# Kernel tuning notes

Measured on AMD Instinct MI355X. Metric: run time of the kernel, lower is better.

Reference implementation:

```python
import jax, jax.numpy as jnp
import numpy as np

B, M, T, D, V = 16, 1024, 4096, 512, 32000
HOPS = 2  # multi_layer_gcn layer_number=2


def setup_inputs() -> dict:
    key = jax.random.key(0)
    ks = jax.random.split(key, 10)
    s = 1.0 / np.sqrt(D)
    emb = jax.random.normal(ks[0], (V, D), jnp.float32) * 0.02
    Ws = jax.random.normal(ks[1], (HOPS, D, D), jnp.float32) * s
    Wn = jax.random.normal(ks[2], (HOPS, D, D), jnp.float32) * s
    Wr = jax.random.normal(ks[3], (HOPS, D, D), jnp.float32) * s
    Wt = jax.random.normal(ks[4], (D, 3 * D), jnp.float32) * (1.0 / np.sqrt(3 * D))
    concept_ids = jax.random.randint(ks[5], (B, M), 0, V)
    relation = jax.random.randint(ks[6], (B, T), 0, V)
    head = jax.random.randint(ks[7], (B, T), 0, M)
    tail = jax.random.randint(ks[8], (B, T), 0, M)
    triple_label = jax.random.randint(ks[9], (B, T), -1, 2)  # {-1,0,1}
    return dict(emb=emb, Ws=Ws, Wn=Wn, Wr=Wr, Wt=Wt,
                concept_ids=concept_ids, relation=relation,
                head=head, tail=tail, triple_label=triple_label)


def _forward(emb, Ws, Wn, Wr, Wt, concept_ids, relation, head, tail, triple_label):
    x = emb[concept_ids]        # [B, M, D] node hidden
    rel = emb[relation]         # [B, T, D] relation hidden
    mask = (triple_label != -1).astype(x.dtype)  # [B, T]

    # per-batch scatter_add into M node slots
    scat = jax.vmap(lambda msg, idx: jnp.zeros((M, msg.shape[-1]), msg.dtype).at[idx].add(msg))
    scat1 = jax.vmap(lambda v, idx: jnp.zeros((M,), v.dtype).at[idx].add(v))

    for i in range(HOPS):
        oh = jnp.take_along_axis(x, head[..., None], axis=1) * mask[..., None]  # gather heads
        ot = jnp.take_along_axis(x, tail[..., None], axis=1) * mask[..., None]  # gather tails
        relm = rel * mask[..., None]
        # update_node += scatter(head_repr - rel -> tail) + scatter(tail_repr - rel -> head)
        upd = scat(oh - relm, tail) + scat(ot - relm, head)          # [B, M, D]
        cnt = scat1(mask, tail) + scat1(mask, head)                  # [B, M]
        x = jax.nn.relu(
            jnp.einsum('bmd,ed->bme', x, Ws[i])
            + jnp.einsum('bmd,ed->bme', upd, Wn[i]) / jnp.maximum(cnt, 1.0)[..., None]
        )
        rel = jnp.einsum('btd,ed->bte', rel, Wr[i])

    head_repr = jnp.take_along_axis(x, head[..., None], axis=1)  # [B, T, D]
    tail_repr = jnp.take_along_axis(x, tail[..., None], axis=1)  # [B, T, D]
    triple_repr = jnp.concatenate([head_repr, rel, tail_repr], axis=-1)  # [B, T, 3D]
    triple_repr = jnp.einsum('btk,dk->btd', triple_repr, Wt)     # [B, T, D]
    encoded_cause = triple_repr.sum(axis=1)                      # [B, D]
    return triple_repr, encoded_cause


def reference(emb, Ws, Wn, Wr, Wt, concept_ids, relation, head, tail, triple_label):
    return _forward(emb, Ws, Wn, Wr, Wt, concept_ids, relation, head, tail, triple_label)
```

## Files before the change

kernel.cpp:

```cpp
#include <hip/hip_runtime.h>

namespace {

constexpr int kB = 16;
constexpr int kM = 1024;
constexpr int kT = 4096;
constexpr int kD = 512;
constexpr int kV = 32000;

typedef __attribute__((ext_vector_type(8))) short bfrag8;
typedef __attribute__((ext_vector_type(4))) float f4acc;

__device__ __forceinline__ ushort f2bf(float f) {
  unsigned u = __float_as_uint(f);
  u += 0x7fffu + ((u >> 16) & 1u);
  return (ushort)(u >> 16);
}
__device__ __forceinline__ float bf2f(ushort h) {
  return __uint_as_float(((unsigned)h) << 16);
}

__device__ __forceinline__ void gload_lds16(const void* g, void* l) {
  __builtin_amdgcn_global_load_lds(
      (const __attribute__((address_space(1))) void*)g,
      (__attribute__((address_space(3))) void*)l, 16, 0, 0);
}

constexpr int kN0 = kV * kD / 4;
constexpr int kN1 = kN0 + 2 * kD * kD / 4;
constexpr int kN2 = kN1 + 2 * kD * kD / 4;
constexpr int kN3 = kN2 + kD * 1536 / 4;
constexpr int kN4 = kN3 + kB * kM * 128;
constexpr int kPREPB = kN4 / 1024;
constexpr int kCSRB = 16;
constexpr int kMM2B = 256;

__global__ __launch_bounds__(1024) void fused_prep_k(
    const float4* __restrict__ emb, const float4* __restrict__ Ws,
    const float4* __restrict__ Wn, const float4* __restrict__ Wt,
    const float* __restrict__ Wnf, const float* __restrict__ Wtf,
    const float* __restrict__ Wrf,
    const int* __restrict__ cid,
    const int* __restrict__ headp, const int* __restrict__ tailp,
    const int* __restrict__ lblp,
    ushort4* __restrict__ EMBb, ushort4* __restrict__ Wsb,
    ushort4* __restrict__ Wnb, ushort4* __restrict__ Wtb,
    ushort4* __restrict__ X0,
    int* __restrict__ deg, int* __restrict__ rowstart, int* __restrict__ epack,
    ushort* __restrict__ Wn2r, float* __restrict__ T1)
{
  __shared__ __align__(16) char shm[12288];
  const int bid = blockIdx.x;
  const int tid = threadIdx.x;

  if (bid < kCSRB) {
    int* sdeg = (int*)shm;
    int* sscan = (int*)(shm + 4096);
    int* sfill = (int*)(shm + 8192);
    const int b = bid;
    sdeg[tid] = 0;
    __syncthreads();
    const int* hb = headp + (b << 12);
    const int* tb = tailp + (b << 12);
    const int* lb = lblp + (b << 12);
    for (int t = tid; t < kT; t += 1024) {
      if (lb[t] == -1) continue;
      atomicAdd(&sdeg[tb[t]], 1);
      atomicAdd(&sdeg[hb[t]], 1);
    }
    __syncthreads();
    int d = sdeg[tid];
    sscan[tid] = d;
    __syncthreads();
    for (int off = 1; off < kM; off <<= 1) {
      int add = (tid >= off) ? sscan[tid - off] : 0;
      __syncthreads();
      sscan[tid] += add;
      __syncthreads();
    }
    int rs = b * (2 * kT) + sscan[tid] - d;
    deg[(b << 10) + tid] = d;
    rowstart[(b << 10) + tid] = rs;
    sfill[tid] = rs;
    __syncthreads();
    for (int t = tid; t < kT; t += 1024) {
      if (lb[t] == -1) continue;
      int hd = hb[t];
      int tl = tb[t];
      int p0 = atomicAdd(&sfill[tl], 1);
      epack[p0] = ((t * 2) << 10) | hd;
      int p1 = atomicAdd(&sfill[hd], 1);
      epack[p1] = ((t * 2 + 1) << 10) | tl;
    }
    __syncthreads();
    for (int i = 1; i < d; ++i) {
      int key = epack[rs + i];
      int j = i - 1;
      while (j >= 0 && epack[rs + j] > key) {
        epack[rs + j + 1] = epack[rs + j];
        --j;
      }
      epack[rs + j + 1] = key;
    }
  } else if (bid < kCSRB + kPREPB) {
    int i = (bid - kCSRB) * 1024 + tid;
    if (i >= kN4) return;
    const float4* s;
    ushort4* dP;
    int off;
    if (i < kN0) { s = emb; dP = EMBb; off = i; }
    else if (i < kN1) { s = Ws; dP = Wsb; off = i - kN0; }
    else if (i < kN2) { s = Wn; dP = Wnb; off = i - kN1; }
    else if (i < kN3) { s = Wt; dP = Wtb; off = i - kN2; }
    else {
      int idx = i - kN3;
      int row = idx >> 7;
      int c = idx & 127;
      float4 v = emb[(size_t)cid[row] * 128 + c];
      ushort4 o;
      o.x = f2bf(v.x); o.y = f2bf(v.y); o.z = f2bf(v.z); o.w = f2bf(v.w);
      X0[idx] = o;
      return;
    }
    float4 v = s[off];
    ushort4 o;
    o.x = f2bf(v.x); o.y = f2bf(v.y); o.z = f2bf(v.z); o.w = f2bf(v.w);
    dP[off] = o;
  } else {
    float (*prow)[512] = (float(*)[512])shm;
    const int mb = bid - kCSRB - kPREPB;
    const int job = mb >> 7;
    const int e0 = (mb & 127) * 4;
    const int k = tid & 511;
    const float* P;
    int strideP, offsP;
    const float* Q;
    if (job == 0) { P = Wnf + (size_t)kD * kD; strideP = 512; offsP = 0; Q = Wrf; }
    else { P = Wtf; strideP = 1536; offsP = 512; Q = Wrf + (size_t)kD * kD; }
    if (tid < 512) {
#pragma unroll
      for (int i = 0; i < 4; ++i)
        prow[i][k] = P[(size_t)(e0 + i) * strideP + offsP + k];
    }
    __syncthreads();
    if (tid < 512) {
      float acc[4] = {0.f, 0.f, 0.f, 0.f};
      for (int a = 0; a < 512; ++a) {
        float qv = Q[a * 512 + k];
#pragma unroll
        for (int i = 0; i < 4; ++i) acc[i] = fmaf(prow[i][a], qv, acc[i]);
      }
#pragma unroll
      for (int i = 0; i < 4; ++i) {
        if (job == 0) Wn2r[(e0 + i) * 512 + k] = f2bf(acc[i]);
        else T1[(e0 + i) * 512 + k] = acc[i];
      }
    }
  }
}

constexpr int kFOLDB = 128;

__global__ __launch_bounds__(512) void fold_aggxr_k(
    const float* __restrict__ T1, const float* __restrict__ Wrf,
    ushort* __restrict__ Wfold,
    const ushort4* __restrict__ Xv, const ushort4* __restrict__ EMBv,
    const int* __restrict__ relid,
    const int* __restrict__ deg, const int* __restrict__ rowstart,
    const int* __restrict__ epack,
    ushort4* __restrict__ SxC, ushort4* __restrict__ nSr0n)
{
  __shared__ float prow[4][512];
  const int bid = blockIdx.x;
  const int tid = threadIdx.x;
  if (bid < kFOLDB) {
    int e0 = bid * 4;
    int k = tid;
#pragma unroll
    for (int i = 0; i < 4; ++i)
      prow[i][k] = T1[(size_t)(e0 + i) * 512 + k];
    __syncthreads();
    float acc[4] = {0.f, 0.f, 0.f, 0.f};
    for (int a = 0; a < 512; ++a) {
      float qv = Wrf[a * 512 + k];
#pragma unroll
      for (int i = 0; i < 4; ++i) acc[i] = fmaf(prow[i][a], qv, acc[i]);
    }
#pragma unroll
    for (int i = 0; i < 4; ++i) Wfold[(e0 + i) * 512 + k] = f2bf(acc[i]);
  } else {
    int bm = (bid - kFOLDB) * 4 + (tid >> 7);
    int t128 = tid & 127;
    int b = bm >> 10;
    int dg = deg[bm];
    int rs = rowstart[bm];
    const int* rid = relid + (b << 12);
    size_t xbase = (size_t)b * kM * 128;
    float ax = 0.f, ay = 0.f, az = 0.f, aw = 0.f;
    float rx = 0.f, ry = 0.f, rz = 0.f, rw = 0.f;
    int e = 0;
    for (; e + 4 <= dg; e += 4) {
      int pk[4];
#pragma unroll
      for (int j = 0; j < 4; ++j) pk[j] = epack[rs + e + j];
      ushort4 xv[4], rv[4];
#pragma unroll
      for (int j = 0; j < 4; ++j) {
        xv[j] = Xv[xbase + (size_t)(pk[j] & 1023) * 128 + t128];
        rv[j] = EMBv[(size_t)rid[pk[j] >> 11] * 128 + t128];
      }
#pragma unroll
      for (int j = 0; j < 4; ++j) {
        ax += bf2f(xv[j].x); ay += bf2f(xv[j].y);
        az += bf2f(xv[j].z); aw += bf2f(xv[j].w);
        rx += bf2f(rv[j].x); ry += bf2f(rv[j].y);
        rz += bf2f(rv[j].z); rw += bf2f(rv[j].w);
      }
    }
    for (; e < dg; ++e) {
      int pk = epack[rs + e];
      ushort4 xv = Xv[xbase + (size_t)(pk & 1023) * 128 + t128];
      ushort4 rv = EMBv[(size_t)rid[pk >> 11] * 128 + t128];
      ax += bf2f(xv.x); ay += bf2f(xv.y); az += bf2f(xv.z); aw += bf2f(xv.w);
      rx += bf2f(rv.x); ry += bf2f(rv.y); rz += bf2f(rv.z); rw += bf2f(rv.w);
    }
    float s = 1.0f / (float)(dg > 0 ? dg : 1);
    ushort4 o;
    o.x = f2bf((ax - rx) * s); o.y = f2bf((ay - ry) * s);
    o.z = f2bf((az - rz) * s); o.w = f2bf((aw - rw) * s);
    SxC[(size_t)bm * 128 + t128] = o;
    o.x = f2bf(-rx * s); o.y = f2bf(-ry * s);
    o.z = f2bf(-rz * s); o.w = f2bf(-rw * s);
    nSr0n[(size_t)bm * 128 + t128] = o;
  }
}

__global__ __launch_bounds__(128) void agg_x_k(
    const ushort4* __restrict__ Xv,
    const int* __restrict__ deg, const int* __restrict__ rowstart,
    const int* __restrict__ epack, ushort4* __restrict__ outv)
{
  int bm = blockIdx.x;
  int b = bm >> 10;
  int tid = threadIdx.x;
  int dg = deg[bm];
  int rs = rowstart[bm];
  size_t xbase = (size_t)b * kM * 128;
  float ax = 0.f, ay = 0.f, az = 0.f, aw = 0.f;
  int e = 0;
  for (; e + 4 <= dg; e += 4) {
    int pk[4];
#pragma unroll
    for (int j = 0; j < 4; ++j) pk[j] = epack[rs + e + j];
    ushort4 xv[4];
#pragma unroll
    for (int j = 0; j < 4; ++j)
      xv[j] = Xv[xbase + (size_t)(pk[j] & 1023) * 128 + tid];
#pragma unroll
    for (int j = 0; j < 4; ++j) {
      ax += bf2f(xv[j].x); ay += bf2f(xv[j].y);
      az += bf2f(xv[j].z); aw += bf2f(xv[j].w);
    }
  }
  for (; e < dg; ++e) {
    int src = epack[rs + e] & 1023;
    ushort4 xv = Xv[xbase + (size_t)src * 128 + tid];
    ax += bf2f(xv.x); ay += bf2f(xv.y); az += bf2f(xv.z); aw += bf2f(xv.w);
  }
  float s = 1.0f / (float)(dg > 0 ? dg : 1);
  ushort4 o;
  o.x = f2bf(ax * s); o.y = f2bf(ay * s); o.z = f2bf(az * s); o.w = f2bf(aw * s);
  outv[(size_t)bm * 128 + tid] = o;
}

template<int MODE>
__global__ __launch_bounds__(256) void gemm_k(
    const ushort* __restrict__ A0, const ushort* __restrict__ A1,
    const ushort* __restrict__ A2,
    const ushort* __restrict__ W1, const ushort* __restrict__ W2,
    const ushort* __restrict__ W3,
    ushort* __restrict__ outbf)
{
  constexpr int NSEG = (MODE == 0) ? 3 : (MODE == 1) ? 2 : 1;
  constexpr bool RELU = (MODE == 0) || (MODE == 1);
  constexpr int NC = (MODE == 4) ? 8 : 4;
  constexpr int OSTR = (MODE == 4) ? 1024 : 512;
  constexpr bool SWZ = (MODE != 5);

  __shared__ __align__(16) char lds[32768];
  char* ldsA = lds;
  char* ldsB = lds + 16384;
  const int tid = threadIdx.x;
  const int w = tid >> 6;
  const int l = tid & 63;
  const int wr = w >> 1;
  const int wc = w & 1;
  const int bid = blockIdx.x;
  int panel, col;
  if constexpr (SWZ) {
    int xcd = bid & 7;
    int idx = bid >> 3;
    panel = xcd * (((int)gridDim.x >> 3) / NC) + idx / NC;
    col = idx % NC;
  } else {
    panel = bid >> 2;
    col = bid & 3;
  }
  const int rowBase = panel * 128;
  const int colBase = col * 128;

  f4acc acc[4][4];
#pragma unroll
  for (int i = 0; i < 4; ++i)
#pragma unroll
    for (int j = 0; j < 4; ++j) acc[i][j] = (f4acc)(0.f);

  int lrow[4], gc[4];
#pragma unroll
  for (int i = 0; i < 4; ++i) {
    int P = (i * 4 + w) * 64 + l;
    lrow[i] = P >> 3;
    gc[i] = (P & 7) ^ (lrow[i] & 7);
  }

  for (int seg = 0; seg < NSEG; ++seg) {
    const char* aP[4];
    const char* bP[4];
#pragma unroll
    for (int i = 0; i < 4; ++i) {
      int grow = rowBase + lrow[i];
      const ushort* ab;
      if constexpr (MODE == 0) {
        ab = (seg == 0 ? A0 : (seg == 1 ? A1 : A2)) + (size_t)grow * kD;
      } else if constexpr (MODE == 1) {
        ab = (seg == 0 ? A0 : A1) + (size_t)grow * kD;
      } else {
        ab = A0 + (size_t)grow * kD;
      }
      aP[i] = (const char*)ab + gc[i] * 16;
      int e = colBase + lrow[i];
      const ushort* wb;
      if constexpr (MODE == 0) {
        wb = (seg == 0 ? W1 : (seg == 1 ? W2 : W3)) + (size_t)e * kD;
      } else if constexpr (MODE == 1) {
        wb = (seg == 0 ? W1 : W2) + (size_t)e * kD;
      } else if constexpr (MODE == 4) {
        wb = W1 + (size_t)(e & 511) * 1536 + (e >> 9) * 1024;
      } else {
        wb = W1 + (size_t)e * kD;
      }
      bP[i] = (const char*)wb + gc[i] * 16;
    }
    for (int kcl = 0; kcl < 8; ++kcl) {
      __syncthreads();
#pragma unroll
      for (int i = 0; i < 4; ++i) {
        gload_lds16(aP[i] + kcl * 128, ldsA + (i * 4 + w) * 1024);
        gload_lds16(bP[i] + kcl * 128, ldsB + (i * 4 + w) * 1024);
      }
      __syncthreads();
#pragma unroll
      for (int ksub = 0; ksub < 2; ++ksub) {
        bfrag8 ef[4], wf[4];
#pragma unroll
        for (int mi = 0; mi < 4; ++mi) {
          int r = wr * 64 + mi * 16 + (l & 15);
          int g = (ksub * 4 + (l >> 4)) ^ (r & 7);
          ef[mi] = *(const bfrag8*)(ldsA + r * 128 + g * 16);
        }
#pragma unroll
        for (int ni = 0; ni < 4; ++ni) {
          int e = wc * 64 + ni * 16 + (l & 15);
          int g = (ksub * 4 + (l >> 4)) ^ (e & 7);
          wf[ni] = *(const bfrag8*)(ldsB + e * 128 + g * 16);
        }
#pragma unroll
        for (int mi = 0; mi < 4; ++mi)
#pragma unroll
          for (int ni = 0; ni < 4; ++ni)
            acc[mi][ni] = __builtin_amdgcn_mfma_f32_16x16x32_bf16(
                wf[ni], ef[mi], acc[mi][ni], 0, 0, 0);
      }
    }
  }

#pragma unroll
  for (int mi = 0; mi < 4; ++mi) {
    int rr = rowBase + wr * 64 + mi * 16 + (l & 15);
#pragma unroll
    for (int ni = 0; ni < 4; ++ni) {
      int cc0 = colBase + wc * 64 + ni * 16 + (l >> 4) * 4;
      float v0 = acc[mi][ni][0], v1 = acc[mi][ni][1];
      float v2 = acc[mi][ni][2], v3 = acc[mi][ni][3];
      if constexpr (RELU) {
        v0 = fmaxf(v0, 0.f); v1 = fmaxf(v1, 0.f);
        v2 = fmaxf(v2, 0.f); v3 = fmaxf(v3, 0.f);
      }
      ushort4 o;
      o.x = f2bf(v0); o.y = f2bf(v1); o.z = f2bf(v2); o.w = f2bf(v3);
      *(ushort4*)(outbf + (size_t)rr * OSTR + cc0) = o;
    }
  }
}

__global__ __launch_bounds__(128) void final_add_k(
    const ushort4* __restrict__ REL2v, const ushort4* __restrict__ HTv,
    const int* __restrict__ relid, const int* __restrict__ headp,
    const int* __restrict__ tailp,
    float* __restrict__ outf, float* __restrict__ part)
{
  const int blk = blockIdx.x;
  const int tid = threadIdx.x;
  const int r0 = blk * 32;
  float cs0 = 0.f, cs1 = 0.f, cs2 = 0.f, cs3 = 0.f;
  for (int i = 0; i < 32; i += 8) {
    ushort4 rv[8], hv[8], tv[8];
#pragma unroll
    for (int j = 0; j < 8; ++j) {
      int r = r0 + i + j;
      int bb = r >> 12;
      rv[j] = REL2v[(size_t)relid[r] * 128 + tid];
      hv[j] = HTv[((size_t)(bb << 10) + headp[r]) * 256 + tid];
      tv[j] = HTv[((size_t)(bb << 10) + tailp[r]) * 256 + 128 + tid];
    }
#pragma unroll
    for (int j = 0; j < 8; ++j) {
      float4 ov;
      ov.x = bf2f(rv[j].x) + bf2f(hv[j].x) + bf2f(tv[j].x);
      ov.y = bf2f(rv[j].y) + bf2f(hv[j].y) + bf2f(tv[j].y);
      ov.z = bf2f(rv[j].z) + bf2f(hv[j].z) + bf2f(tv[j].z);
      ov.w = bf2f(rv[j].w) + bf2f(hv[j].w) + bf2f(tv[j].w);
      cs0 += ov.x; cs1 += ov.y; cs2 += ov.z; cs3 += ov.w;
      *(float4*)(outf + (size_t)(r0 + i + j) * 512 + tid * 4) = ov;
    }
  }
  float4 o; o.x = cs0; o.y = cs1; o.z = cs2; o.w = cs3;
  *(float4*)(part + (size_t)blk * 512 + tid * 4) = o;
}

__global__ __launch_bounds__(512) void reduce_enc_k(
    const float* __restrict__ part, float* __restrict__ enc)
{
  int b = blockIdx.x;
  int c = threadIdx.x;
  float s = 0.f;
  for (int rt = 0; rt < 128; ++rt) s += part[(size_t)(b * 128 + rt) * 512 + c];
  enc[b * 512 + c] = s;
}

}

extern "C" void kernel_launch(void* const* d_in, const int* in_sizes, int n_in,
                              void* d_out, int out_size, void* d_ws, size_t ws_size,
                              hipStream_t stream) {
  const float* emb = (const float*)d_in[0];
  const float* Ws = (const float*)d_in[1];
  const float* Wn = (const float*)d_in[2];
  const float* Wr = (const float*)d_in[3];
  const float* Wt = (const float*)d_in[4];
  const int* cid = (const int*)d_in[5];
  const int* relid = (const int*)d_in[6];
  const int* headp = (const int*)d_in[7];
  const int* tailp = (const int*)d_in[8];
  const int* lblp = (const int*)d_in[9];
  float* out = (float*)d_out;

  char* wsp = (char*)d_ws;
  ushort* EMBb  = (ushort*)(wsp);
  ushort* HT    = (ushort*)(wsp);
  ushort* REL2  = (ushort*)(wsp + (32ull << 20));
  ushort* Wsb   = (ushort*)(wsp + (64ull << 20));
  ushort* Wnb   = (ushort*)(wsp + (65ull << 20));
  ushort* Wtb   = (ushort*)(wsp + (66ull << 20));
  ushort* Wn2r  = (ushort*)(wsp + (67ull << 20) + (512ull << 10));
  ushort* Wfold = (ushort*)(wsp + (68ull << 20));
  float*  T1    = (float*)(wsp + (68ull << 20) + (512ull << 10));
  int* deg      = (int*)(wsp + (70ull << 20));
  int* rowstart = deg + kB * kM;
  int* epack    = rowstart + kB * kM;
  float* part   = (float*)(wsp + (71ull << 20));

  char* outc = (char*)d_out;
  ushort* X0    = (ushort*)(outc);
  ushort* Sxn   = (ushort*)(outc + (16ull << 20));
  ushort* nSr0n = (ushort*)(outc + (32ull << 20));
  ushort* X1    = (ushort*)(outc + (48ull << 20));
  ushort* X2    = X0;
  float* ENC = out + (size_t)kB * kT * kD;

  fused_prep_k<<<kCSRB + kPREPB + kMM2B, 1024, 0, stream>>>(
      (const float4*)emb, (const float4*)Ws, (const float4*)Wn,
      (const float4*)Wt, Wn, Wt, Wr, cid, headp, tailp, lblp,
      (ushort4*)EMBb, (ushort4*)Wsb, (ushort4*)Wnb, (ushort4*)Wtb,
      (ushort4*)X0, deg, rowstart, epack, Wn2r, T1);

  fold_aggxr_k<<<kFOLDB + kB * kM / 4, 512, 0, stream>>>(
      T1, Wr, Wfold, (const ushort4*)X0, (const ushort4*)EMBb, relid,
      deg, rowstart, epack, (ushort4*)Sxn, (ushort4*)nSr0n);

  gemm_k<1><<<(kB * kM / 128) * 4, 256, 0, stream>>>(
      X0, Sxn, nullptr, Wsb, Wnb, nullptr, X1);

  gemm_k<5><<<(kV / 128) * 4, 256, 0, stream>>>(
      EMBb, nullptr, nullptr, Wfold, nullptr, nullptr, REL2);

  agg_x_k<<<kB * kM, 128, 0, stream>>>(
      (const ushort4*)X1, deg, rowstart, epack, (ushort4*)Sxn);

  gemm_k<0><<<(kB * kM / 128) * 4, 256, 0, stream>>>(
      X1, Sxn, nSr0n, Wsb + (size_t)kD * kD, Wnb + (size_t)kD * kD, Wn2r, X2);

  gemm_k<4><<<(kB * kM / 128) * 8, 256, 0, stream>>>(
      X2, nullptr, nullptr, Wtb, nullptr, nullptr, HT);

  final_add_k<<<kB * kT / 32, 128, 0, stream>>>(
      (const ushort4*)REL2, (const ushort4*)HT, relid, headp, tailp, out, part);

  reduce_enc_k<<<kB, 512, 0, stream>>>(part, ENC);
}
```

Baseline: 273.6 us.

## Build CSR edge lists in LDS and merge two independent GEMM launches

The CSR-building blocks now scatter and insertion-sort the per-batch edge list in shared memory, then copy it to global memory in one coalesced pass. Before, each scatter and sort step read and wrote global memory. The hop-1 node GEMM and the relation-fold GEMM are also merged into one launch that dispatches on block index, which removes a launch gap and lets the two independent GEMMs run concurrently. The prep kernel's shared memory grows to about 44 KB, which may lower occupancy for its other block roles.

```diff
diff --git a/kernel.cpp b/kernel.cpp
--- a/kernel.cpp
+++ b/kernel.cpp
@@ -49,7 +49,7 @@
     int* __restrict__ deg, int* __restrict__ rowstart, int* __restrict__ epack,
     ushort* __restrict__ Wn2r, float* __restrict__ T1)
 {
-  __shared__ __align__(16) char shm[12288];
+  __shared__ __align__(16) char shm[45056];
   const int bid = blockIdx.x;
   const int tid = threadIdx.x;
 
@@ -57,6 +57,7 @@
     int* sdeg = (int*)shm;
     int* sscan = (int*)(shm + 4096);
     int* sfill = (int*)(shm + 8192);
+    int* sep = (int*)(shm + 12288);
     const int b = bid;
     sdeg[tid] = 0;
     __syncthreads();
@@ -78,30 +79,33 @@
       sscan[tid] += add;
       __syncthreads();
     }
-    int rs = b * (2 * kT) + sscan[tid] - d;
+    int lrs = sscan[tid] - d;
     deg[(b << 10) + tid] = d;
-    rowstart[(b << 10) + tid] = rs;
-    sfill[tid] = rs;
+    rowstart[(b << 10) + tid] = b * (2 * kT) + lrs;
+    sfill[tid] = lrs;
     __syncthreads();
     for (int t = tid; t < kT; t += 1024) {
       if (lb[t] == -1) continue;
       int hd = hb[t];
       int tl = tb[t];
       int p0 = atomicAdd(&sfill[tl], 1);
-      epack[p0] = ((t * 2) << 10) | hd;
+      sep[p0] = ((t * 2) << 10) | hd;
       int p1 = atomicAdd(&sfill[hd], 1);
-      epack[p1] = ((t * 2 + 1) << 10) | tl;
+      sep[p1] = ((t * 2 + 1) << 10) | tl;
     }
     __syncthreads();
     for (int i = 1; i < d; ++i) {
-      int key = epack[rs + i];
+      int key = sep[lrs + i];
       int j = i - 1;
-      while (j >= 0 && epack[rs + j] > key) {
-        epack[rs + j + 1] = epack[rs + j];
+      while (j >= 0 && sep[lrs + j] > key) {
+        sep[lrs + j + 1] = sep[lrs + j];
         --j;
       }
-      epack[rs + j + 1] = key;
-    }
+      sep[lrs + j + 1] = key;
+    }
+    __syncthreads();
+    for (int i = tid; i < 2 * kT; i += 1024)
+      epack[b * (2 * kT) + i] = sep[i];
   } else if (bid < kCSRB + kPREPB) {
     int i = (bid - kCSRB) * 1024 + tid;
     if (i >= kN4) return;
@@ -274,7 +278,8 @@
 }
 
 template<int MODE>
-__global__ __launch_bounds__(256) void gemm_k(
+__device__ __forceinline__ void gemm_body(
+    char* lds, int bid, int nblocks,
     const ushort* __restrict__ A0, const ushort* __restrict__ A1,
     const ushort* __restrict__ A2,
     const ushort* __restrict__ W1, const ushort* __restrict__ W2,
@@ -287,7 +292,6 @@
   constexpr int OSTR = (MODE == 4) ? 1024 : 512;
   constexpr bool SWZ = (MODE != 5);
 
-  __shared__ __align__(16) char lds[32768];
   char* ldsA = lds;
   char* ldsB = lds + 16384;
   const int tid = threadIdx.x;
@@ -295,12 +299,11 @@
   const int l = tid & 63;
   const int wr = w >> 1;
   const int wc = w & 1;
-  const int bid = blockIdx.x;
   int panel, col;
   if constexpr (SWZ) {
     int xcd = bid & 7;
     int idx = bid >> 3;
-    panel = xcd * (((int)gridDim.x >> 3) / NC) + idx / NC;
+    panel = xcd * ((nblocks >> 3) / NC) + idx / NC;
     col = idx % NC;
   } else {
     panel = bid >> 2;
@@ -401,6 +404,35 @@
       *(ushort4*)(outbf + (size_t)rr * OSTR + cc0) = o;
     }
   }
+}
+
+template<int MODE>
+__global__ __launch_bounds__(256) void gemm_k(
+    const ushort* __restrict__ A0, const ushort* __restrict__ A1,
+    const ushort* __restrict__ A2,
+    const ushort* __restrict__ W1, const ushort* __restrict__ W2,
+    const ushort* __restrict__ W3,
+    ushort* __restrict__ outbf)
+{
+  __shared__ __align__(16) char lds[32768];
+  gemm_body<MODE>(lds, blockIdx.x, gridDim.x, A0, A1, A2, W1, W2, W3, outbf);
+}
+
+constexpr int kH1B = (kB * kM / 128) * 4;
+
+__global__ __launch_bounds__(256) void gemm_h1r2_k(
+    const ushort* __restrict__ X0, const ushort* __restrict__ SxC,
+    const ushort* __restrict__ Wsb, const ushort* __restrict__ Wnb,
+    ushort* __restrict__ X1,
+    const ushort* __restrict__ EMBb, const ushort* __restrict__ Wfold,
+    ushort* __restrict__ REL2)
+{
+  __shared__ __align__(16) char lds[32768];
+  if (blockIdx.x < kH1B)
+    gemm_body<1>(lds, blockIdx.x, kH1B, X0, SxC, nullptr, Wsb, Wnb, nullptr, X1);
+  else
+    gemm_body<5>(lds, blockIdx.x - kH1B, (kV / 128) * 4, EMBb, nullptr, nullptr,
+                 Wfold, nullptr, nullptr, REL2);
 }
 
 __global__ __launch_bounds__(128) void final_add_k(
@@ -498,11 +530,8 @@
       T1, Wr, Wfold, (const ushort4*)X0, (const ushort4*)EMBb, relid,
       deg, rowstart, epack, (ushort4*)Sxn, (ushort4*)nSr0n);
 
-  gemm_k<1><<<(kB * kM / 128) * 4, 256, 0, stream>>>(
-      X0, Sxn, nullptr, Wsb, Wnb, nullptr, X1);
-
-  gemm_k<5><<<(kV / 128) * 4, 256, 0, stream>>>(
-      EMBb, nullptr, nullptr, Wfold, nullptr, nullptr, REL2);
+  gemm_h1r2_k<<<kH1B + (kV / 128) * 4, 256, 0, stream>>>(
+      X0, Sxn, Wsb, Wnb, X1, EMBb, Wfold, REL2);
 
   agg_x_k<<<kB * kM, 128, 0, stream>>>(
       (const ushort4*)X1, deg, rowstart, epack, (ushort4*)Sxn);
```

Measured after the change: 284.6 us. 4.0% more time.
